# Performance work log

Measured on AMD Instinct MI355X. Metric: run time of the kernel, lower is better.

The kernel has to match this reference:

```python
import jax, jax.numpy as jnp
import numpy as np

S, L, D = 128, 512, 256   # MSA rows, residues, msa_dim
H, C = 8, 32              # num_heads, head_dim


def setup_inputs() -> dict:
    key = jax.random.key(0)
    ks = jax.random.split(key, 8)
    inp = {
        "msa_input": jax.random.normal(ks[0], (S, L, D), dtype=jnp.float32),
        "ln_scale": jnp.ones((D,), jnp.float32),
        "ln_bias": jnp.zeros((D,), jnp.float32),
        "wq": jax.random.normal(ks[1], (D, H * C), jnp.float32) / np.sqrt(D),
        "wk": jax.random.normal(ks[2], (D, H * C), jnp.float32) / np.sqrt(D),
        "wv": jax.random.normal(ks[3], (D, H * C), jnp.float32) / np.sqrt(D),
        "wg": jax.random.normal(ks[4], (D, H * C), jnp.float32) / np.sqrt(D),
        "bg": jnp.zeros((H * C,), jnp.float32),
        "wo": jax.random.normal(ks[5], (H * C, D), jnp.float32) / np.sqrt(H * C),
        "bo": jnp.zeros((D,), jnp.float32),
    }
    return inp


def reference(msa_input, ln_scale, ln_bias, wq, wk, wv, wg, bg, wo, bo):
    # LayerNorm over last dim (eps matches torch default 1e-5)
    mu = jnp.mean(msa_input, axis=-1, keepdims=True)
    var = jnp.mean(jnp.square(msa_input - mu), axis=-1, keepdims=True)
    x = (msa_input - mu) * jax.lax.rsqrt(var + 1e-5) * ln_scale + ln_bias

    q = (x @ wq).reshape(S, L, H, C)
    k = (x @ wk).reshape(S, L, H, C)
    v = (x @ wv).reshape(S, L, H, C)
    g = jax.nn.sigmoid(x @ wg + bg).reshape(S, L, H, C)

    scale = 1.0 / np.sqrt(C)
    # attention over MSA-row axis, per residue l and head h
    scores = jnp.einsum("slhc,tlhc->stlh", q, k) * scale   # [S,S,L,H]
    probs = jax.nn.softmax(scores, axis=1)                  # softmax over t
    o = jnp.einsum("stlh,tlhc->slhc", probs, v) * g         # [S,L,H,C]
    return o.reshape(S, L, H * C) @ wo + bo
```

## Files before the change

### kernel.cpp

```cpp
#include <hip/hip_runtime.h>
#include <hip/hip_bf16.h>

typedef __bf16 bf16;
typedef __bf16 bf16x8 __attribute__((ext_vector_type(8)));
typedef float f32x4 __attribute__((ext_vector_type(4)));

#define S_DIM 128
#define L_DIM 512
#define D_DIM 256
#define NQ    1024

__device__ __forceinline__ void gl16(void* lds, const void* g) {
  __builtin_amdgcn_global_load_lds((const __attribute__((address_space(1))) void*)g,
                                   (__attribute__((address_space(3))) void*)lds,
                                   16, 0, 0);
}

__global__ void pack_weights(const float* __restrict__ wq, const float* __restrict__ wk,
                             const float* __restrict__ wv, const float* __restrict__ wg,
                             const float* __restrict__ wo,
                             bf16* __restrict__ wcat_t, bf16* __restrict__ wo_t) {
  int idx = blockIdx.x * 256 + threadIdx.x;
  const int total1 = NQ * D_DIM;
  if (idx < total1) {
    int j = idx >> 8;
    int d = idx & 255;
    const float* w = (j < 256) ? wq : (j < 512) ? wk : (j < 768) ? wv : wg;
    wcat_t[idx] = (bf16)w[d * 256 + (j & 255)];
  } else {
    int i2 = idx - total1;
    if (i2 < D_DIM * D_DIM) {
      int dcol = i2 >> 8, k = i2 & 255;
      wo_t[i2] = (bf16)wo[k * 256 + dcol];
    }
  }
}

__global__ __launch_bounds__(256) void ln_kernel(const float* __restrict__ x,
                                                 const float* __restrict__ sc,
                                                 const float* __restrict__ bs,
                                                 bf16* __restrict__ y) {
  int wid  = threadIdx.x >> 6;
  int lane = threadIdx.x & 63;
  int row  = blockIdx.x * 4 + wid;
  float4 v = ((const float4*)(x + (size_t)row * D_DIM))[lane];
  float s = v.x + v.y + v.z + v.w;
  #pragma unroll
  for (int m = 32; m; m >>= 1) s += __shfl_xor(s, m);
  float mu = s * (1.0f / 256.0f);
  float dx = v.x - mu, dy = v.y - mu, dz = v.z - mu, dw = v.w - mu;
  float s2 = dx * dx + dy * dy + dz * dz + dw * dw;
  #pragma unroll
  for (int m = 32; m; m >>= 1) s2 += __shfl_xor(s2, m);
  float rs = rsqrtf(s2 * (1.0f / 256.0f) + 1e-5f);
  float4 scv = ((const float4*)sc)[lane];
  float4 bsv = ((const float4*)bs)[lane];
  union { uint2 u; bf16 b[4]; } o;
  o.b[0] = (bf16)(dx * rs * scv.x + bsv.x);
  o.b[1] = (bf16)(dy * rs * scv.y + bsv.y);
  o.b[2] = (bf16)(dz * rs * scv.z + bsv.z);
  o.b[3] = (bf16)(dw * rs * scv.w + bsv.w);
  ((uint2*)y)[(size_t)row * 64 + lane] = o.u;
}

__device__ __forceinline__ bf16x8 lds_swz(const bf16* base, int row, int k) {
  return *(const bf16x8*)((const char*)base + ((((row << 6) + k) << 1) ^ ((row & 7) << 4)));
}

__global__ __launch_bounds__(256, 4) void gemm_qkvg(const bf16* __restrict__ A,
                                                    const bf16* __restrict__ Bt,
                                                    bf16* __restrict__ Cout,
                                                    const float* __restrict__ bias) {
  __shared__ __align__(16) bf16 smem[16384];
  bf16* As = smem;
  bf16* Bs = smem + 8192;
  const int tid  = threadIdx.x;
  const int wid  = tid >> 6;
  const int lane = tid & 63;
  const int bid   = blockIdx.x;
  const int n_idx = (bid >> 3) & 7;
  const int m_idx = (bid & 7) | ((bid >> 6) << 3);
  const int m0 = m_idx * 128;
  const int n0 = n_idx * 128;
  const int lrow = lane & 15;
  const int lk   = (lane >> 4) * 8;
  const int wr = wid >> 1, wc = wid & 1;

  const int ln8 = lane >> 3;
  const int c8  = ((lane & 7) ^ ln8) * 8;

  const bf16* Arow = A  + (size_t)m0 * 256 + c8;
  const bf16* Brow = Bt + (size_t)n0 * 256 + c8;

  f32x4 acc[4][4] = {};

  #pragma unroll
  for (int ks = 0; ks < 4; ++ks) {
    const int k0 = ks * 64;
    #pragma unroll
    for (int t = 0; t < 4; ++t) {
      int chunk = wid * 4 + t;
      int r = chunk * 8 + ln8;
      gl16(&As[chunk * 512], Arow + (size_t)r * 256 + k0);
      gl16(&Bs[chunk * 512], Brow + (size_t)r * 256 + k0);
    }
    __syncthreads();
    #pragma unroll
    for (int kk = 0; kk < 64; kk += 32) {
      bf16x8 av[4], bv[4];
      #pragma unroll
      for (int i = 0; i < 4; ++i)
        av[i] = lds_swz(As, wr * 64 + i * 16 + lrow, kk + lk);
      #pragma unroll
      for (int j = 0; j < 4; ++j)
        bv[j] = lds_swz(Bs, wc * 64 + j * 16 + lrow, kk + lk);
      #pragma unroll
      for (int i = 0; i < 4; ++i)
        #pragma unroll
        for (int j = 0; j < 4; ++j)
          acc[i][j] = __builtin_amdgcn_mfma_f32_16x16x32_bf16(av[i], bv[j], acc[i][j], 0, 0, 0);
    }
    __syncthreads();
  }

  const int rb = (lane >> 4) * 4;
  const int xorv = rb << 2;

  const bool isg = (n0 >= 768);
  float bgv[4];
  if (isg) {
    #pragma unroll
    for (int j = 0; j < 4; ++j) bgv[j] = bias[n0 - 768 + wc * 64 + j * 16 + lrow];
  }
  #pragma unroll
  for (int i = 0; i < 4; ++i)
    #pragma unroll
    for (int j = 0; j < 4; ++j) {
      int col = wc * 64 + j * 16 + lrow;
      #pragma unroll
      for (int r = 0; r < 4; ++r) {
        int row = wr * 64 + i * 16 + rb + r;
        float v = acc[i][j][r];
        if (isg) { v += bgv[j]; v = 1.0f / (1.0f + __expf(-v)); }
        smem[row * 128 + (col ^ xorv)] = (bf16)v;
      }
    }
  __syncthreads();
  #pragma unroll
  for (int p = 0; p < 8; ++p) {
    int chunk = p * 256 + tid;
    int row = chunk >> 4, slot8 = (chunk & 15) * 8;
    int rx = (row & 12) << 2;
    *(uint4*)(Cout + (size_t)(m0 + row) * NQ + n0 + slot8) =
        *(const uint4*)(smem + row * 128 + (slot8 ^ rx));
  }
}

__global__ __launch_bounds__(512) void attn_proj(const bf16* __restrict__ qkvg,
                                                 const bf16* __restrict__ wo_t,
                                                 const float* __restrict__ bo,
                                                 float* __restrict__ out) {
  __shared__ __align__(16) bf16 q_s[128 * 32];
  __shared__ __align__(16) bf16 k_s[128 * 32];
  __shared__ __align__(16) bf16 vt_s[32 * 136];
  __shared__ __align__(16) char p_rg[34816];
  bf16*  p_s = (bf16*)p_rg;
  bf16*  w_s = (bf16*)p_rg;
  float* f_b = (float*)p_rg;

  const int tid  = threadIdx.x;
  const int wid  = tid >> 6;
  const int lane = tid & 63;
  const int lrow = lane & 15;
  const int lk   = (lane >> 4) * 8;
  const int rb   = (lane >> 4) * 4;
  const int res  = blockIdx.x;

  const int wm = wid >> 1;
  const int wn = wid & 1;
  const int s0 = wid * 16;

  float bov[8];
  #pragma unroll
  for (int j = 0; j < 8; ++j) bov[j] = bo[wn * 128 + j * 16 + lrow];

  f32x4 acc[2][8] = {};

  const int srow = (wid * 64 + lane) >> 2;
  const int sslot = lane & 3;

  for (int h = 0; h < 8; ++h) {
    const int hc0 = h * 32;
    {
      const bf16* src = qkvg + ((size_t)srow * L_DIM + res) * NQ + hc0 + sslot * 8;
      gl16(q_s + wid * 512, src);
      gl16(k_s + wid * 512, src + 256);
      int row = tid >> 2, slot = tid & 3;
      union { uint4 u; bf16 e[8]; } v;
      v.u = *(const uint4*)(qkvg + ((size_t)row * L_DIM + res) * NQ + 512 + hc0 + slot * 8);
      #pragma unroll
      for (int j = 0; j < 8; ++j) vt_s[(slot * 8 + j) * 136 + row] = v.e[j];
    }
    __syncthreads();

    f32x4 s8[8];
    {
      const f32x4 z = {0.f, 0.f, 0.f, 0.f};
      bf16x8 av = *(const bf16x8*)(q_s + (s0 + lrow) * 32 + lk);
      #pragma unroll
      for (int tc = 0; tc < 8; ++tc) {
        bf16x8 bv = *(const bf16x8*)(k_s + (tc * 16 + lrow) * 32 + lk);
        s8[tc] = __builtin_amdgcn_mfma_f32_16x16x32_bf16(av, bv, z, 0, 0, 0);
      }
    }
    const float scale = 0.17677669529663687f;
    #pragma unroll
    for (int r = 0; r < 4; ++r) {
      float m = -1e30f;
      #pragma unroll
      for (int tc = 0; tc < 8; ++tc) m = fmaxf(m, s8[tc][r]);
      #pragma unroll
      for (int msk = 8; msk; msk >>= 1) m = fmaxf(m, __shfl_xor(m, msk));
      float pv[8], ssum = 0.f;
      #pragma unroll
      for (int tc = 0; tc < 8; ++tc) {
        float p = __expf((s8[tc][r] - m) * scale);
        pv[tc] = p; ssum += p;
      }
      #pragma unroll
      for (int msk = 8; msk; msk >>= 1) ssum += __shfl_xor(ssum, msk);
      float inv = 1.0f / ssum;
      int prow = s0 + rb + r;
      #pragma unroll
      for (int tc = 0; tc < 8; ++tc)
        p_s[prow * 136 + tc * 16 + lrow] = (bf16)(pv[tc] * inv);
    }

    f32x4 oc[2] = {};
    #pragma unroll
    for (int kc = 0; kc < 4; ++kc) {
      bf16x8 pa = *(const bf16x8*)(p_s + (s0 + lrow) * 136 + kc * 32 + lk);
      bf16x8 b0 = *(const bf16x8*)(vt_s + lrow * 136 + kc * 32 + lk);
      bf16x8 b1 = *(const bf16x8*)(vt_s + (16 + lrow) * 136 + kc * 32 + lk);
      oc[0] = __builtin_amdgcn_mfma_f32_16x16x32_bf16(pa, b0, oc[0], 0, 0, 0);
      oc[1] = __builtin_amdgcn_mfma_f32_16x16x32_bf16(pa, b1, oc[1], 0, 0, 0);
    }
    #pragma unroll
    for (int cj = 0; cj < 2; ++cj)
      #pragma unroll
      for (int r = 0; r < 4; ++r)
        q_s[(s0 + rb + r) * 32 + cj * 16 + lrow] = (bf16)oc[cj][r];
    __syncthreads();

    #pragma unroll
    for (int t = 0; t < 2; ++t) {
      int ch = t * 512 + wid * 64 + lane;
      int row = ch >> 2, slot = ch & 3;
      gl16((char*)p_rg + (t * 512 + wid * 64) * 16, wo_t + row * 256 + hc0 + slot * 8);
    }
    {
      int row = tid >> 2, slot = tid & 3;
      union { uint4 u; bf16 e[8]; } g, o;
      g.u = *(const uint4*)(qkvg + ((size_t)row * L_DIM + res) * NQ + 768 + hc0 + slot * 8);
      o.u = *(const uint4*)(q_s + row * 32 + slot * 8);
      #pragma unroll
      for (int j = 0; j < 8; ++j) o.e[j] = (bf16)((float)o.e[j] * (float)g.e[j]);
      *(uint4*)(q_s + row * 32 + slot * 8) = o.u;
    }
    __syncthreads();

    {
      bf16x8 av0 = *(const bf16x8*)(q_s + (wm * 32 + lrow) * 32 + lk);
      bf16x8 av1 = *(const bf16x8*)(q_s + (wm * 32 + 16 + lrow) * 32 + lk);
      #pragma unroll
      for (int j = 0; j < 8; ++j) {
        bf16x8 bv = *(const bf16x8*)(w_s + (wn * 128 + j * 16 + lrow) * 32 + lk);
        acc[0][j] = __builtin_amdgcn_mfma_f32_16x16x32_bf16(av0, bv, acc[0][j], 0, 0, 0);
        acc[1][j] = __builtin_amdgcn_mfma_f32_16x16x32_bf16(av1, bv, acc[1][j], 0, 0, 0);
      }
    }
    __syncthreads();
  }

  #pragma unroll 1
  for (int b = 0; b < 4; ++b) {
    if (wm == b) {
      #pragma unroll
      for (int i = 0; i < 2; ++i)
        #pragma unroll
        for (int j = 0; j < 8; ++j)
          #pragma unroll
          for (int r = 0; r < 4; ++r) {
            int br = i * 16 + rb + r;
            int col = wn * 128 + j * 16 + lrow;
            f_b[br * 256 + (col ^ ((br & 12) << 2))] = acc[i][j][r] + bov[j];
          }
    }
    __syncthreads();
    #pragma unroll
    for (int u = 0; u < 4; ++u) {
      int ch = u * 512 + tid;
      int br = ch >> 6, slot = ch & 63;
      int phys = (slot * 4) ^ ((br & 12) << 2);
      *(uint4*)(out + ((size_t)(b * 32 + br) * L_DIM + res) * 256 + slot * 4) =
          *(const uint4*)(f_b + br * 256 + phys);
    }
    __syncthreads();
  }
}

extern "C" void kernel_launch(void* const* d_in, const int* in_sizes, int n_in,
                              void* d_out, int out_size, void* d_ws, size_t ws_size,
                              hipStream_t stream) {
  const float* msa      = (const float*)d_in[0];
  const float* ln_scale = (const float*)d_in[1];
  const float* ln_bias  = (const float*)d_in[2];
  const float* wq       = (const float*)d_in[3];
  const float* wk       = (const float*)d_in[4];
  const float* wv       = (const float*)d_in[5];
  const float* wg       = (const float*)d_in[6];
  const float* bg       = (const float*)d_in[7];
  const float* wo       = (const float*)d_in[8];
  const float* bo       = (const float*)d_in[9];
  float* out = (float*)d_out;

  char* ws = (char*)d_ws;
  bf16* wcat_t = (bf16*)ws;
  bf16* wo_t   = (bf16*)(ws + 524288);
  bf16* qkvg   = (bf16*)(ws + 655360);
  bf16* x_ln   = (bf16*)d_out;

  pack_weights<<<dim3(1280), dim3(256), 0, stream>>>(wq, wk, wv, wg, wo, wcat_t, wo_t);
  ln_kernel<<<dim3(65536 / 4), dim3(256), 0, stream>>>(msa, ln_scale, ln_bias, x_ln);
  gemm_qkvg<<<dim3(4096), dim3(256), 0, stream>>>(x_ln, wcat_t, qkvg, bg);
  attn_proj<<<dim3(512), dim3(512), 0, stream>>>(qkvg, wo_t, bo, out);
}
```

Baseline: 164.4 us.

## Assign one head per wave in attention kernel, drop per-head block barriers

The attention+projection kernel now gives each of the 8 waves its own head: K fragments stay in registers, Q is loaded straight from global, and V is transposed into a per-wave LDS slice. The probabilities go through a small per-wave LDS buffer, so the per-head __syncthreads loop is gone. Gated outputs for all heads are gathered into one LDS tile, and the output projection then runs in two halves over a swizzled full-K Wo tile. In exchange the kernel needs a much larger LDS allocation (~152KB), which limits occupancy to one block per CU and raises register pressure.

Result: faster. 156.9 us (-4.5%).

```diff
diff --git a/kernel.cpp b/kernel.cpp
--- a/kernel.cpp
+++ b/kernel.cpp
@@ -160,150 +160,165 @@
                                                  const bf16* __restrict__ wo_t,
                                                  const float* __restrict__ bo,
                                                  float* __restrict__ out) {
-  __shared__ __align__(16) bf16 q_s[128 * 32];
-  __shared__ __align__(16) bf16 k_s[128 * 32];
-  __shared__ __align__(16) bf16 vt_s[32 * 136];
-  __shared__ __align__(16) char p_rg[34816];
-  bf16*  p_s = (bf16*)p_rg;
-  bf16*  w_s = (bf16*)p_rg;
-  float* f_b = (float*)p_rg;
-
+  __shared__ __align__(16) char smem[155648];
   const int tid  = threadIdx.x;
   const int wid  = tid >> 6;
   const int lane = tid & 63;
   const int lrow = lane & 15;
-  const int lk   = (lane >> 4) * 8;
-  const int rb   = (lane >> 4) * 4;
+  const int lkg  = lane >> 4;
+  const int lk   = lkg * 8;
+  const int rb   = lkg * 4;
   const int res  = blockIdx.x;
-
-  const int wm = wid >> 1;
-  const int wn = wid & 1;
-  const int s0 = wid * 16;
-
-  float bov[8];
-  #pragma unroll
-  for (int j = 0; j < 8; ++j) bov[j] = bo[wn * 128 + j * 16 + lrow];
-
-  f32x4 acc[2][8] = {};
-
-  const int srow = (wid * 64 + lane) >> 2;
-  const int sslot = lane & 3;
-
-  for (int h = 0; h < 8; ++h) {
-    const int hc0 = h * 32;
-    {
-      const bf16* src = qkvg + ((size_t)srow * L_DIM + res) * NQ + hc0 + sslot * 8;
-      gl16(q_s + wid * 512, src);
-      gl16(k_s + wid * 512, src + 256);
-      int row = tid >> 2, slot = tid & 3;
+  const int hc0  = wid * 32;
+
+  bf16* vw = (bf16*)smem + wid * (32 * 136);
+  bf16* pw = (bf16*)(smem + 69632) + wid * (16 * 72);
+  bf16* of = (bf16*)(smem + 88064);
+
+  {
+    int t0 = lane >> 2, cs = (lane & 3) * 8;
+    #pragma unroll
+    for (int pass = 0; pass < 8; ++pass) {
+      int t = pass * 16 + t0;
       union { uint4 u; bf16 e[8]; } v;
-      v.u = *(const uint4*)(qkvg + ((size_t)row * L_DIM + res) * NQ + 512 + hc0 + slot * 8);
-      #pragma unroll
-      for (int j = 0; j < 8; ++j) vt_s[(slot * 8 + j) * 136 + row] = v.e[j];
-    }
-    __syncthreads();
-
-    f32x4 s8[8];
-    {
-      const f32x4 z = {0.f, 0.f, 0.f, 0.f};
-      bf16x8 av = *(const bf16x8*)(q_s + (s0 + lrow) * 32 + lk);
-      #pragma unroll
-      for (int tc = 0; tc < 8; ++tc) {
-        bf16x8 bv = *(const bf16x8*)(k_s + (tc * 16 + lrow) * 32 + lk);
-        s8[tc] = __builtin_amdgcn_mfma_f32_16x16x32_bf16(av, bv, z, 0, 0, 0);
-      }
-    }
-    const float scale = 0.17677669529663687f;
+      v.u = *(const uint4*)(qkvg + (size_t)(t * L_DIM + res) * NQ + 512 + hc0 + cs);
+      #pragma unroll
+      for (int j = 0; j < 8; ++j) vw[(cs + j) * 136 + t] = v.e[j];
+    }
+  }
+
+  bf16x8 kf[8];
+  #pragma unroll
+  for (int tt = 0; tt < 8; ++tt)
+    kf[tt] = *(const bf16x8*)(qkvg + (size_t)((tt * 16 + lrow) * L_DIM + res) * NQ + 256 + hc0 + lk);
+
+  const float scale = 0.17677669529663687f;
+  const f32x4 z = {0.f, 0.f, 0.f, 0.f};
+
+  for (int st = 0; st < 8; ++st) {
+    bf16x8 qf = *(const bf16x8*)(qkvg + (size_t)((st * 16 + lrow) * L_DIM + res) * NQ + hc0 + lk);
+    f32x4 sc[8];
+    #pragma unroll
+    for (int tt = 0; tt < 8; ++tt)
+      sc[tt] = __builtin_amdgcn_mfma_f32_16x16x32_bf16(qf, kf[tt], z, 0, 0, 0);
+
     #pragma unroll
     for (int r = 0; r < 4; ++r) {
-      float m = -1e30f;
-      #pragma unroll
-      for (int tc = 0; tc < 8; ++tc) m = fmaxf(m, s8[tc][r]);
+      float m = sc[0][r];
+      #pragma unroll
+      for (int tc = 1; tc < 8; ++tc) m = fmaxf(m, sc[tc][r]);
       #pragma unroll
       for (int msk = 8; msk; msk >>= 1) m = fmaxf(m, __shfl_xor(m, msk));
       float pv[8], ssum = 0.f;
       #pragma unroll
       for (int tc = 0; tc < 8; ++tc) {
-        float p = __expf((s8[tc][r] - m) * scale);
+        float p = __expf((sc[tc][r] - m) * scale);
         pv[tc] = p; ssum += p;
       }
       #pragma unroll
       for (int msk = 8; msk; msk >>= 1) ssum += __shfl_xor(ssum, msk);
       float inv = 1.0f / ssum;
-      int prow = s0 + rb + r;
-      #pragma unroll
-      for (int tc = 0; tc < 8; ++tc)
-        p_s[prow * 136 + tc * 16 + lrow] = (bf16)(pv[tc] * inv);
-    }
-
-    f32x4 oc[2] = {};
-    #pragma unroll
-    for (int kc = 0; kc < 4; ++kc) {
-      bf16x8 pa = *(const bf16x8*)(p_s + (s0 + lrow) * 136 + kc * 32 + lk);
-      bf16x8 b0 = *(const bf16x8*)(vt_s + lrow * 136 + kc * 32 + lk);
-      bf16x8 b1 = *(const bf16x8*)(vt_s + (16 + lrow) * 136 + kc * 32 + lk);
-      oc[0] = __builtin_amdgcn_mfma_f32_16x16x32_bf16(pa, b0, oc[0], 0, 0, 0);
-      oc[1] = __builtin_amdgcn_mfma_f32_16x16x32_bf16(pa, b1, oc[1], 0, 0, 0);
-    }
-    #pragma unroll
-    for (int cj = 0; cj < 2; ++cj)
+      #pragma unroll
+      for (int tc = 0; tc < 8; ++tc) sc[tc][r] = pv[tc] * inv;
+    }
+
+    f32x4 oc[2] = {z, z};
+    #pragma unroll
+    for (int hf = 0; hf < 2; ++hf) {
+      #pragma unroll
+      for (int tc = 0; tc < 4; ++tc)
+        #pragma unroll
+        for (int r = 0; r < 4; ++r)
+          pw[(rb + r) * 72 + tc * 16 + lrow] = (bf16)sc[hf * 4 + tc][r];
+      #pragma unroll
+      for (int kc = 0; kc < 2; ++kc) {
+        bf16x8 pa = *(const bf16x8*)(pw + lrow * 72 + kc * 32 + lk);
+        #pragma unroll
+        for (int ct = 0; ct < 2; ++ct) {
+          bf16x8 bv = *(const bf16x8*)(vw + (ct * 16 + lrow) * 136 + hf * 64 + kc * 32 + lk);
+          oc[ct] = __builtin_amdgcn_mfma_f32_16x16x32_bf16(pa, bv, oc[ct], 0, 0, 0);
+        }
+      }
+    }
+    #pragma unroll
+    for (int ct = 0; ct < 2; ++ct)
       #pragma unroll
       for (int r = 0; r < 4; ++r)
-        q_s[(s0 + rb + r) * 32 + cj * 16 + lrow] = (bf16)oc[cj][r];
-    __syncthreads();
-
-    #pragma unroll
-    for (int t = 0; t < 2; ++t) {
-      int ch = t * 512 + wid * 64 + lane;
-      int row = ch >> 2, slot = ch & 3;
-      gl16((char*)p_rg + (t * 512 + wid * 64) * 16, wo_t + row * 256 + hc0 + slot * 8);
-    }
-    {
-      int row = tid >> 2, slot = tid & 3;
-      union { uint4 u; bf16 e[8]; } g, o;
-      g.u = *(const uint4*)(qkvg + ((size_t)row * L_DIM + res) * NQ + 768 + hc0 + slot * 8);
-      o.u = *(const uint4*)(q_s + row * 32 + slot * 8);
-      #pragma unroll
-      for (int j = 0; j < 8; ++j) o.e[j] = (bf16)((float)o.e[j] * (float)g.e[j]);
-      *(uint4*)(q_s + row * 32 + slot * 8) = o.u;
-    }
-    __syncthreads();
-
-    {
-      bf16x8 av0 = *(const bf16x8*)(q_s + (wm * 32 + lrow) * 32 + lk);
-      bf16x8 av1 = *(const bf16x8*)(q_s + (wm * 32 + 16 + lrow) * 32 + lk);
-      #pragma unroll
-      for (int j = 0; j < 8; ++j) {
-        bf16x8 bv = *(const bf16x8*)(w_s + (wn * 128 + j * 16 + lrow) * 32 + lk);
-        acc[0][j] = __builtin_amdgcn_mfma_f32_16x16x32_bf16(av0, bv, acc[0][j], 0, 0, 0);
-        acc[1][j] = __builtin_amdgcn_mfma_f32_16x16x32_bf16(av1, bv, acc[1][j], 0, 0, 0);
+        of[(st * 16 + rb + r) * 264 + hc0 + ct * 16 + lrow] = (bf16)oc[ct][r];
+  }
+  __syncthreads();
+
+  const int pbase = (wid >> 1) * 32;
+  const int pn    = wid & 1;
+
+  bf16x8 af[2][8];
+  #pragma unroll
+  for (int mt = 0; mt < 2; ++mt) {
+    int s = pbase + mt * 16 + lrow;
+    #pragma unroll
+    for (int kt = 0; kt < 8; ++kt) {
+      bf16x8 o8 = *(const bf16x8*)(of + s * 264 + kt * 32 + lk);
+      bf16x8 g8 = *(const bf16x8*)(qkvg + (size_t)(s * L_DIM + res) * NQ + 768 + kt * 32 + lk);
+      bf16x8 rr;
+      #pragma unroll
+      for (int j = 0; j < 8; ++j) rr[j] = (bf16)((float)o8[j] * (float)g8[j]);
+      af[mt][kt] = rr;
+    }
+  }
+
+  float bov[2][4];
+  #pragma unroll
+  for (int hf = 0; hf < 2; ++hf)
+    #pragma unroll
+    for (int nt = 0; nt < 4; ++nt)
+      bov[hf][nt] = bo[hf * 128 + pn * 64 + nt * 16 + lrow];
+
+  bf16* wS = (bf16*)smem;
+  f32x4 acc[2][2][4] = {};
+  #pragma unroll
+  for (int hf = 0; hf < 2; ++hf) {
+    #pragma unroll
+    for (int pass = 0; pass < 8; ++pass) {
+      int ch = pass * 512 + tid;
+      int dl = ch >> 5, sl = ch & 31;
+      gl16((char*)wS + (pass * 512 + wid * 64) * 16,
+           wo_t + (size_t)(hf * 128 + dl) * 256 + (sl ^ (dl & 7)) * 8);
+    }
+    __syncthreads();
+    #pragma unroll
+    for (int kt = 0; kt < 8; ++kt)
+      #pragma unroll
+      for (int nt = 0; nt < 4; ++nt) {
+        int dl = pn * 64 + nt * 16 + lrow;
+        bf16x8 bw = *(const bf16x8*)((char*)wS + dl * 512 + (((kt * 4 + lkg) ^ (dl & 7)) * 16));
+        acc[hf][0][nt] = __builtin_amdgcn_mfma_f32_16x16x32_bf16(af[0][kt], bw, acc[hf][0][nt], 0, 0, 0);
+        acc[hf][1][nt] = __builtin_amdgcn_mfma_f32_16x16x32_bf16(af[1][kt], bw, acc[hf][1][nt], 0, 0, 0);
       }
-    }
-    __syncthreads();
-  }
-
+    __syncthreads();
+  }
+
+  float* fb = (float*)smem;
   #pragma unroll 1
   for (int b = 0; b < 4; ++b) {
-    if (wm == b) {
-      #pragma unroll
-      for (int i = 0; i < 2; ++i)
+    if ((wid >> 1) == b) {
+      #pragma unroll
+      for (int hf = 0; hf < 2; ++hf)
         #pragma unroll
-        for (int j = 0; j < 8; ++j)
+        for (int mt = 0; mt < 2; ++mt)
           #pragma unroll
-          for (int r = 0; r < 4; ++r) {
-            int br = i * 16 + rb + r;
-            int col = wn * 128 + j * 16 + lrow;
-            f_b[br * 256 + (col ^ ((br & 12) << 2))] = acc[i][j][r] + bov[j];
-          }
+          for (int nt = 0; nt < 4; ++nt)
+            #pragma unroll
+            for (int r = 0; r < 4; ++r)
+              fb[(mt * 16 + rb + r) * 264 + hf * 128 + pn * 64 + nt * 16 + lrow] =
+                  acc[hf][mt][nt][r] + bov[hf][nt];
     }
     __syncthreads();
     #pragma unroll
     for (int u = 0; u < 4; ++u) {
       int ch = u * 512 + tid;
-      int br = ch >> 6, slot = ch & 63;
-      int phys = (slot * 4) ^ ((br & 12) << 2);
-      *(uint4*)(out + ((size_t)(b * 32 + br) * L_DIM + res) * 256 + slot * 4) =
-          *(const uint4*)(f_b + br * 256 + phys);
+      int row = ch >> 6, c4 = (ch & 63) * 4;
+      *(uint4*)(out + (size_t)((b * 32 + row) * L_DIM + res) * 256 + c4) =
+          *(const uint4*)(fb + row * 264 + c4);
     }
     __syncthreads();
   }
```
